# Kernel optimization log

Hardware: AMD Instinct MI355X
Metric: run time of the kernel (lower is better)

The kernel has to match this reference:

```python
import jax, jax.numpy as jnp
import numpy as np

N = 50000      # nodes
E = 800000     # edges (avg degree 16)
F_IN = 128     # num_features
H = 64         # hidden_dim
G = 64         # graphs in batch


def setup_inputs() -> dict:
    key = jax.random.key(0)
    ks = jax.random.split(key, 20)
    inp = {
        "x": jax.random.normal(ks[0], (N, F_IN), jnp.float32),
        "edge_index": jax.random.randint(ks[1], (2, E), 0, N, dtype=jnp.int32).astype(jnp.int64),
        "batch": jnp.sort(jax.random.randint(ks[2], (N,), 0, G, dtype=jnp.int32)).astype(jnp.int64),
    }
    # GraphConv layer dims: in -> out
    dims = [(F_IN, H), (H, 2 * H), (2 * H, 3 * H), (3 * H, H)]
    k = 3
    for i, (din, dout) in enumerate(dims):
        s = 1.0 / np.sqrt(din).astype(np.float32)
        inp[f"w{i+1}_rel"] = jax.random.normal(ks[k], (din, dout), jnp.float32) * s
        inp[f"w{i+1}_root"] = jax.random.normal(ks[k + 1], (din, dout), jnp.float32) * s
        inp[f"b{i+1}"] = jnp.zeros((dout,), jnp.float32)
        k += 2
    inp["head_w"] = jax.random.normal(ks[k], (H, 1), jnp.float32) * (1.0 / np.sqrt(H).astype(np.float32))
    inp["head_b"] = jnp.zeros((1,), jnp.float32)
    return inp


def _graph_conv(x, src, dst, w_rel, w_root, b):
    # PyG GraphConv: out = lin_rel(sum_{j in N(i)} x_j) + lin_root(x_i)
    agg = jax.ops.segment_sum(x[src], dst, num_segments=N)  # [N, din]
    return agg @ w_rel + b + x @ w_root


def reference(x, edge_index, batch,
              w1_rel, w1_root, b1,
              w2_rel, w2_root, b2,
              w3_rel, w3_root, b3,
              w4_rel, w4_root, b4,
              head_w, head_b):
    src, dst = edge_index[0], edge_index[1]
    h = jax.nn.relu(_graph_conv(x, src, dst, w1_rel, w1_root, b1))
    h = jax.nn.relu(_graph_conv(h, src, dst, w2_rel, w2_root, b2))
    h = jax.nn.relu(_graph_conv(h, src, dst, w3_rel, w3_root, b3))
    h = _graph_conv(h, src, dst, w4_rel, w4_root, b4)          # [N, H]
    # global_mean_pool over graph ids
    sums = jax.ops.segment_sum(h, batch, num_segments=G)       # [G, H]
    counts = jax.ops.segment_sum(jnp.ones((N,), h.dtype), batch, num_segments=G)
    pooled = sums / jnp.maximum(counts, 1.0)[:, None]          # [G, H]
    return pooled @ head_w + head_b                            # [G, 1]
```

## Files before the change

### kernel.cpp

```cpp
#include <hip/hip_runtime.h>


#define NNODES 50000
#define NEDGES 800000
#define NGRAPH 64
#define NBUK 256
#define BSZ 196
#define EPB (NEDGES / NBUK)
#define CVT_NB (NNODES * 128 / 4 / 256)
#define PACK_NB (160 * 512 / 256)
#define PREP_NB (CVT_NB + PACK_NB + 1)
#define RGRID ((NNODES + 127) / 128)
#define RCHUNK ((RGRID + 7) / 8)
#define GB_SPLIT 196
#define ZNB 32

typedef __attribute__((ext_vector_type(8))) __bf16 bf16x8;
typedef __attribute__((ext_vector_type(16))) float f32x16;

__device__ __forceinline__ unsigned short f2bf(float f) {
    unsigned u = __float_as_uint(f);
    u += 0x7fff + ((u >> 16) & 1);
    return (unsigned short)(u >> 16);
}
__device__ __forceinline__ float bf2f(unsigned b) {
    return __uint_as_float(b << 16);
}

__device__ __forceinline__ void dma16(const void* g, void* l) {
    __builtin_amdgcn_global_load_lds(
        (const __attribute__((address_space(1))) void*)g,
        (__attribute__((address_space(3))) void*)l, 16, 0, 0);
}


__device__ __forceinline__ void pack32(const float* __restrict__ W, unsigned short* __restrict__ dst,
                                       int KS_tot, int ks0, int dcols, int ct0,
                                       int tl, int ksl, int lane, int j) {
    int k = ksl * 16 + ((lane >> 5) << 3) + j;
    int col = tl * 32 + (lane & 31);
    dst[(((size_t)(ct0 + tl) * KS_tot + (ks0 + ksl)) * 64 + lane) * 8 + j] = f2bf(W[k * dcols + col]);
}

__device__ void prep_body(int b, int tid,
                          const float* x, unsigned short* xbf,
                          const float* w1_rel, const float* w1_root,
                          const float* w2_rel, const float* w2_root,
                          const float* w3_rel, const float* w3_root,
                          unsigned short* pL1, unsigned short* pL2, unsigned short* pL3,
                          const float* w4_rel, const float* w4_root,
                          const float* b4, const float* head_w,
                          float* wr, float* wt, float* cbuf) {
    if (b < CVT_NB) {
        int i = b * 256 + tid;
        float4 v = ((const float4*)x)[i];
        unsigned lo = (unsigned)f2bf(v.x) | ((unsigned)f2bf(v.y) << 16);
        unsigned hi = (unsigned)f2bf(v.z) | ((unsigned)f2bf(v.w) << 16);
        ((uint2*)xbf)[i] = make_uint2(lo, hi);
    } else if (b < CVT_NB + PACK_NB) {
        int idx = (b - CVT_NB) * 256 + tid;
        int g = idx >> 9;
        int t = idx & 511;
        int lane = (t >> 3) & 63, j = t & 7;
        if (g < 16)       { int gl = g;       pack32(w1_rel,  pL1, 8,  0, 64,  0, gl / 8, gl % 8, lane, j); }
        else if (g < 32)  { int gl = g - 16;  pack32(w1_root, pL1, 8,  0, 64,  2, gl / 8, gl % 8, lane, j); }
        else if (g < 48)  { int gl = g - 32;  pack32(w2_rel,  pL2, 8,  0, 128, 0, gl / 4, gl % 4, lane, j); }
        else if (g < 64)  { int gl = g - 48;  pack32(w2_root, pL2, 8,  4, 128, 0, gl / 4, gl % 4, lane, j); }
        else if (g < 112) { int gl = g - 64;  pack32(w3_rel,  pL3, 16, 0, 192, 0, gl / 8, gl % 8, lane, j); }
        else              { int gl = g - 112; pack32(w3_root, pL3, 16, 8, 192, 0, gl / 8, gl % 8, lane, j); }
    } else {
        if (tid < 192) {
            float ar = 0.f, at = 0.f;
            for (int j = 0; j < 64; j++) {
                float hw = head_w[j];
                ar = fmaf(w4_rel[tid * 64 + j], hw, ar);
                at = fmaf(w4_root[tid * 64 + j], hw, at);
            }
            wr[tid] = ar;
            wt[tid] = at;
        } else if (tid == 192) {
            float c = 0.f;
            for (int j = 0; j < 64; j++) c = fmaf(b4[j], head_w[j], c);
            cbuf[0] = c;
        }
    }
}


__global__ void __launch_bounds__(256) histprep_kernel(
    const int* __restrict__ edst, int* __restrict__ bcnt,
    const float* __restrict__ x, unsigned short* __restrict__ xbf,
    const float* __restrict__ w1_rel, const float* __restrict__ w1_root,
    const float* __restrict__ w2_rel, const float* __restrict__ w2_root,
    const float* __restrict__ w3_rel, const float* __restrict__ w3_root,
    unsigned short* __restrict__ pL1, unsigned short* __restrict__ pL2,
    unsigned short* __restrict__ pL3,
    const float* __restrict__ w4_rel, const float* __restrict__ w4_root,
    const float* __restrict__ b4, const float* __restrict__ head_w,
    float* __restrict__ wr, float* __restrict__ wt, float* __restrict__ cbuf)
{
    int tid = threadIdx.x, b = blockIdx.x;
    if (b < NBUK) {
        __shared__ int h[NBUK];
        h[tid] = 0;
        __syncthreads();
        int end = (b + 1) * EPB;
        for (int i = b * EPB + tid; i < end; i += 256)
            atomicAdd(&h[edst[i] / BSZ], 1);
        __syncthreads();
        bcnt[tid * NBUK + b] = h[tid];
    } else {
        prep_body(b - NBUK, tid, x, xbf, w1_rel, w1_root, w2_rel, w2_root,
                  w3_rel, w3_root, pL1, pL2, pL3, w4_rel, w4_root, b4, head_w,
                  wr, wt, cbuf);
    }
}


__global__ void scanzero_kernel(int* __restrict__ a, int* __restrict__ bsum, int n,
                                float4* __restrict__ zb, int zn16) {
    __shared__ int buf[256];
    int tid = threadIdx.x, b = blockIdx.x;
    if (b < NBUK) {
        int i = b * 256 + tid;
        int v = (i < n) ? a[i] : 0;
        buf[tid] = v;
        __syncthreads();
        #pragma unroll
        for (int off = 1; off < 256; off <<= 1) {
            int t = (tid >= off) ? buf[tid - off] : 0;
            __syncthreads();
            buf[tid] += t;
            __syncthreads();
        }
        if (i < n) a[i] = buf[tid] - v;
        if (tid == 255) bsum[b] = buf[255];
    } else {
        float4 zero = make_float4(0.f, 0.f, 0.f, 0.f);
        for (int i = (b - NBUK) * 256 + tid; i < zn16; i += ZNB * 256) zb[i] = zero;
    }
}


template<int KS, int NT, int NHALF, int ST, int KCH>
__device__ void gemm_body(
    unsigned short* sB, unsigned short* sA, int i,
    const unsigned short* __restrict__ A, const unsigned short* __restrict__ Wall,
    const float* __restrict__ bias, unsigned short* __restrict__ OUT,
    int ldo, int ocol0, int relu, int N,
    const float* __restrict__ wrp, const float* __restrict__ wtp,
    float* __restrict__ sb, float* __restrict__ tb)
{
    const int K = KS * 16;
    const int CPC = KCH * 2;

    int chunk = i / (8 * NHALF);
    int rem = i - chunk * (8 * NHALF);
    int halfsel = rem >> 3;
    int rowb = chunk * 8 + (rem & 7);
    int rbase = rowb * 128;
    if (rbase >= N) return;

    int tid = threadIdx.x;
    int wave = tid >> 6, lane = tid & 63;
    int l32 = lane & 31, half = lane >> 5;
    const unsigned short* W = Wall + (size_t)halfsel * NT * KS * 512;

    #pragma unroll
    for (int j = 0; j < NT * KS * 64 / 256; j++) {
        int p = j * 256 + wave * 64;
        dma16(W + ((size_t)p + lane) * 8, sB + (size_t)p * 8);
    }

    f32x16 acc[NT];
    #pragma unroll
    for (int t = 0; t < NT; t++)
        #pragma unroll
        for (int r = 0; r < 16; r++) acc[t][r] = 0.f;

    int lr = wave * 32 + l32;

    for (int kb = 0; kb < KS; kb += KCH) {
        if (kb > 0) __syncthreads();
        #pragma unroll
        for (int j = 0; j < 128 * CPC / 256; j++) {
            int p = j * 256 + wave * 64 + lane;
            int r = p / CPC;
            int c = p - r * CPC;
            int cg = c ^ (r & (CPC - 1));
            dma16(A + (size_t)(rbase + r) * K + kb * 16 + cg * 8,
                  sA + (size_t)(j * 256 + wave * 64) * 8);
        }
        __syncthreads();
        #pragma unroll
        for (int l = 0; l < KCH; l++) {
            int cs = (l * 2 + half) ^ (lr & (CPC - 1));
            bf16x8 a = *(const bf16x8*)(sA + (size_t)lr * (KCH * 16) + cs * 8);
            int ks = kb + l;
            #pragma unroll
            for (int t = 0; t < NT; t++) {
                bf16x8 b = *(const bf16x8*)(sB + ((size_t)(t * KS + ks) * 64 + lane) * 8);
                acc[t] = __builtin_amdgcn_mfma_f32_32x32x16_bf16(a, b, acc[t], 0, 0, 0);
            }
        }
    }

    int wrbase = rbase + wave * 32;
    if constexpr (ST) {
        #pragma unroll
        for (int reg = 0; reg < 16; reg++) {
            int row = wrbase + (reg & 3) + 8 * (reg >> 2) + 4 * half;
            float sv = 0.f, tv = 0.f;
            #pragma unroll
            for (int t = 0; t < NT; t++) {
                int col = halfsel * NT * 32 + t * 32 + l32;
                float v = fmaxf(acc[t][reg] + bias[col], 0.f);
                sv = fmaf(v, wrp[col], sv);
                tv = fmaf(v, wtp[col], tv);
            }
            #pragma unroll
            for (int m = 1; m < 32; m <<= 1) {
                sv += __shfl_xor(sv, m, 64);
                tv += __shfl_xor(tv, m, 64);
            }
            if (l32 == 0 && row < N) {
                atomicAdd(&sb[row], sv);
                atomicAdd(&tb[row], tv);
            }
        }
    } else {
        #pragma unroll
        for (int t = 0; t < NT; t++) {
            int col = t * 32 + l32;
            float bi = bias ? bias[col] : 0.f;
            #pragma unroll
            for (int reg = 0; reg < 16; reg++) {
                int row = wrbase + (reg & 3) + 8 * (reg >> 2) + 4 * half;
                if (row < N) {
                    float v = acc[t][reg] + bi;
                    if (relu) v = fmaxf(v, 0.f);
                    OUT[(size_t)row * ldo + ocol0 + col] = f2bf(v);
                }
            }
        }
    }
}

template<int KS, int NT, int NHALF, int ST, int KCH>
__global__ __launch_bounds__(256) void gemm_v5(
    const unsigned short* __restrict__ A, const unsigned short* __restrict__ Wall,
    const float* __restrict__ bias, unsigned short* __restrict__ OUT,
    int ldo, int ocol0, int relu, int N,
    const float* __restrict__ wrp, const float* __restrict__ wtp,
    float* __restrict__ sb, float* __restrict__ tb)
{
    __shared__ __align__(16) unsigned short sB[NT * KS * 512];
    __shared__ __align__(16) unsigned short sA[128 * KCH * 16];
    gemm_body<KS, NT, NHALF, ST, KCH>(sB, sA, blockIdx.x, A, Wall, bias, OUT,
                                      ldo, ocol0, relu, N, wrp, wtp, sb, tb);
}


__global__ void __launch_bounds__(256) partgemm_kernel(
    const int* __restrict__ src, const int* __restrict__ dst,
    const int* __restrict__ cnt, const int* __restrict__ braw,
    int* __restrict__ sbsum, unsigned long long* __restrict__ pedge,
    const unsigned short* __restrict__ A, const unsigned short* __restrict__ W,
    unsigned short* __restrict__ OUT, int N)
{
    __shared__ __align__(16) unsigned short smem[32768];
    int tid = threadIdx.x, b = blockIdx.x;
    if (b < NBUK) {
        int* lbase = (int*)smem;
        int* sscan = lbase + 256;
        int v = braw[tid];
        sscan[tid] = v;
        __syncthreads();
        #pragma unroll
        for (int off = 1; off < 256; off <<= 1) {
            int t = (tid >= off) ? sscan[tid - off] : 0;
            __syncthreads();
            sscan[tid] += t;
            __syncthreads();
        }
        int ex = sscan[tid] - v;
        if (b == 0) sbsum[tid] = ex;
        lbase[tid] = cnt[tid * NBUK + b] + ex;
        __syncthreads();
        int end = (b + 1) * EPB;
        for (int i = b * EPB + tid; i < end; i += 256) {
            int s = src[i], d = dst[i];
            int pos = atomicAdd(&lbase[d / BSZ], 1);
            pedge[pos] = (unsigned long long)(unsigned)s | ((unsigned long long)(unsigned)d << 32);
        }
    } else {
        gemm_body<8, 4, 1, 0, 8>(smem, smem + 16384, b - NBUK,
                                 A, W, nullptr, OUT, 128, 0, 0, N,
                                 nullptr, nullptr, nullptr, nullptr);
    }
}


__global__ void __launch_bounds__(256) buildgemm_kernel(
    const unsigned long long* __restrict__ pedge, const int* __restrict__ sbsum,
    int* __restrict__ rp, int* __restrict__ csr,
    const unsigned short* __restrict__ A, const unsigned short* __restrict__ W,
    unsigned short* __restrict__ OUT, int N)
{
    __shared__ __align__(16) unsigned short smem[32768];
    int tid = threadIdx.x, b = blockIdx.x;
    if (b < NBUK) {
        int* sdeg  = (int*)smem;
        int* sc    = sdeg + 256;
        int* sbase = sc + 256;
        int* sfill = sbase + 256;
        int node0 = b * BSZ;
        int ncnt = NNODES - node0;
        if (ncnt > BSZ) ncnt = BSZ;
        if (ncnt < 0) ncnt = 0;
        int seg0 = sbsum[b];
        int seg1 = (b + 1 < NBUK) ? sbsum[b + 1] : NEDGES;
        sdeg[tid] = 0;
        sfill[tid] = 0;
        __syncthreads();
        for (int i = seg0 + tid; i < seg1; i += 256)
            atomicAdd(&sdeg[(int)(pedge[i] >> 32) - node0], 1);
        __syncthreads();
        sc[tid] = sdeg[tid];
        __syncthreads();
        #pragma unroll
        for (int off = 1; off < 256; off <<= 1) {
            int t = (tid >= off) ? sc[tid - off] : 0;
            __syncthreads();
            sc[tid] += t;
            __syncthreads();
        }
        sbase[tid] = sc[tid] - sdeg[tid];
        if (tid < ncnt) rp[node0 + tid] = seg0 + sbase[tid];
        if (b == NBUK - 1 && tid == 0) rp[NNODES] = NEDGES;
        __syncthreads();
        for (int i = seg0 + tid; i < seg1; i += 256) {
            unsigned long long p = pedge[i];
            int d = (int)(p >> 32) - node0;
            int pos = atomicAdd(&sfill[d], 1);
            csr[seg0 + sbase[d] + pos] = (int)(p & 0xffffffffu);
        }
    } else {
        gemm_body<8, 4, 1, 0, 8>(smem, smem + 16384, GB_SPLIT + (b - NBUK),
                                 A, W, nullptr, OUT, 128, 0, 0, N,
                                 nullptr, nullptr, nullptr, nullptr);
    }
}


__device__ __forceinline__ void acc8(float* a, uint4 u) {
    a[0] += bf2f(u.x & 0xffffu); a[1] += bf2f(u.x >> 16);
    a[2] += bf2f(u.y & 0xffffu); a[3] += bf2f(u.y >> 16);
    a[4] += bf2f(u.z & 0xffffu); a[5] += bf2f(u.z >> 16);
    a[6] += bf2f(u.w & 0xffffu); a[7] += bf2f(u.w >> 16);
}

template<int LPF, int SUBS>
__global__ void agg_kernel_v4(const unsigned short* __restrict__ X, int ldx,
                              const int* __restrict__ rp, const int* __restrict__ csr,
                              const unsigned short* __restrict__ root, int ldr,
                              const float* __restrict__ bias, int relu,
                              unsigned short* __restrict__ OUT, int ldo, int N) {
    int t = blockIdx.x * blockDim.x + threadIdx.x;
    int node = t / (SUBS * LPF);
    int r = t % (SUBS * LPF);
    int sub = r / LPF;
    int sl = r % LPF;
    if (node >= N) return;
    float a[8] = {0.f, 0.f, 0.f, 0.f, 0.f, 0.f, 0.f, 0.f};
    int e0 = rp[node], e1 = rp[node + 1];
    const unsigned short* xb = X + 8 * sl;
    int e = e0 + sub;
    for (; e + 3 * SUBS < e1; e += 4 * SUBS) {
        int s0 = csr[e], s1 = csr[e + SUBS], s2 = csr[e + 2 * SUBS], s3 = csr[e + 3 * SUBS];
        uint4 u0 = *(const uint4*)(xb + (size_t)s0 * ldx);
        uint4 u1 = *(const uint4*)(xb + (size_t)s1 * ldx);
        uint4 u2 = *(const uint4*)(xb + (size_t)s2 * ldx);
        uint4 u3 = *(const uint4*)(xb + (size_t)s3 * ldx);
        acc8(a, u0); acc8(a, u1); acc8(a, u2); acc8(a, u3);
    }
    for (; e < e1; e += SUBS) {
        uint4 u = *(const uint4*)(xb + (size_t)csr[e] * ldx);
        acc8(a, u);
    }
    #pragma unroll
    for (int m = LPF; m < SUBS * LPF; m <<= 1)
        #pragma unroll
        for (int i = 0; i < 8; i++) a[i] += __shfl_xor(a[i], m, 64);
    if (sub == 0) {
        if (root) {
            uint4 u = *(const uint4*)(root + (size_t)node * ldr + 8 * sl);
            acc8(a, u);
        }
        if (bias) {
            float4 b0 = *(const float4*)(bias + 8 * sl);
            float4 b1 = *(const float4*)(bias + 8 * sl + 4);
            a[0] += b0.x; a[1] += b0.y; a[2] += b0.z; a[3] += b0.w;
            a[4] += b1.x; a[5] += b1.y; a[6] += b1.z; a[7] += b1.w;
        }
        if (relu) {
            #pragma unroll
            for (int i = 0; i < 8; i++) a[i] = fmaxf(a[i], 0.f);
        }
        uint4 o;
        o.x = (unsigned)f2bf(a[0]) | ((unsigned)f2bf(a[1]) << 16);
        o.y = (unsigned)f2bf(a[2]) | ((unsigned)f2bf(a[3]) << 16);
        o.z = (unsigned)f2bf(a[4]) | ((unsigned)f2bf(a[5]) << 16);
        o.w = (unsigned)f2bf(a[6]) | ((unsigned)f2bf(a[7]) << 16);
        *(uint4*)(OUT + (size_t)node * ldo + 8 * sl) = o;
    }
}


__global__ void aggpool_kernel(const float* __restrict__ s, const float* __restrict__ t,
                               const int* __restrict__ rp, const int* __restrict__ csr,
                               const int* __restrict__ batch, float* __restrict__ gsum,
                               int* __restrict__ cnt, int N) {
    __shared__ float ls[NGRAPH];
    __shared__ int lc[NGRAPH];
    int tid = threadIdx.x;
    if (tid < NGRAPH) { ls[tid] = 0.f; lc[tid] = 0; }
    __syncthreads();
    int n = blockIdx.x * blockDim.x + tid;
    if (n < N) {
        float a = 0.f;
        int e = rp[n], e1 = rp[n + 1];
        for (; e + 3 < e1; e += 4) {
            int s0 = csr[e], s1 = csr[e + 1], s2 = csr[e + 2], s3 = csr[e + 3];
            a += s[s0] + s[s1] + s[s2] + s[s3];
        }
        for (; e < e1; e++) a += s[csr[e]];
        int g = batch[n];
        atomicAdd(&ls[g], a + t[n]);
        atomicAdd(&lc[g], 1);
    }
    __syncthreads();
    if (tid < NGRAPH && lc[tid] > 0) {
        atomicAdd(&gsum[tid], ls[tid]);
        atomicAdd(&cnt[tid], lc[tid]);
    }
}

__global__ void final_kernel(const float* __restrict__ gsum, const int* __restrict__ cnt,
                             const float* __restrict__ cbuf, const float* __restrict__ head_b,
                             float* __restrict__ out) {
    int g = threadIdx.x;
    if (g < NGRAPH) {
        float c = (float)(cnt[g] > 0 ? cnt[g] : 1);
        out[g] = gsum[g] / c + cbuf[0] + head_b[0];
    }
}


extern "C" void kernel_launch(void* const* d_in, const int* in_sizes, int n_in,
                              void* d_out, int out_size, void* d_ws, size_t ws_size,
                              hipStream_t stream) {
    const float* x       = (const float*)d_in[0];
    const int*   edge    = (const int*)d_in[1];
    const int*   batch   = (const int*)d_in[2];
    const float* w1_rel  = (const float*)d_in[3];
    const float* w1_root = (const float*)d_in[4];
    const float* b1      = (const float*)d_in[5];
    const float* w2_rel  = (const float*)d_in[6];
    const float* w2_root = (const float*)d_in[7];
    const float* b2      = (const float*)d_in[8];
    const float* w3_rel  = (const float*)d_in[9];
    const float* w3_root = (const float*)d_in[10];
    const float* b3      = (const float*)d_in[11];
    const float* w4_rel  = (const float*)d_in[12];
    const float* w4_root = (const float*)d_in[13];
    const float* b4      = (const float*)d_in[14];
    const float* head_w  = (const float*)d_in[15];
    const float* head_b  = (const float*)d_in[16];
    float* out = (float*)d_out;

    const int N = NNODES, E = NEDGES;
    const int* esrc = edge;
    const int* edst = edge + E;

    char* ws = (char*)d_ws;
    size_t off = 0;
    auto alloc = [&](size_t bytes) -> char* {
        char* p = ws + off;
        off = (off + bytes + 255) & ~(size_t)255;
        return p;
    };
    float* gsum  = (float*)alloc(NGRAPH * 4);
    int*   cnt   = (int*)alloc(NGRAPH * 4);
    float* sbuf  = (float*)alloc((size_t)N * 4);
    float* tbuf  = (float*)alloc((size_t)N * 4);
    size_t zero_bytes = off;
    int*   bcnt  = (int*)alloc((size_t)NBUK * NBUK * 4);
    int*   bsum  = (int*)alloc(256 * 4);
    int*   sbsum = (int*)alloc(256 * 4);
    int*   rp    = (int*)alloc((size_t)(N + 1) * 4);
    int*   csr   = (int*)alloc((size_t)E * 4);
    unsigned long long* pedge = (unsigned long long*)alloc((size_t)E * 8);
    unsigned short* xbf    = (unsigned short*)alloc((size_t)N * 128 * 2);
    unsigned short* z1     = (unsigned short*)alloc((size_t)N * 128 * 2);
    unsigned short* combo2 = (unsigned short*)alloc((size_t)N * 128 * 2);
    unsigned short* combo3 = (unsigned short*)alloc((size_t)N * 256 * 2);
    unsigned short* pL1    = (unsigned short*)alloc(4 * 8 * 512 * 2);
    unsigned short* pL2    = (unsigned short*)alloc(4 * 8 * 512 * 2);
    unsigned short* pL3    = (unsigned short*)alloc(6 * 16 * 512 * 2);
    float* wr    = (float*)alloc(192 * 4);
    float* wt    = (float*)alloc(192 * 4);
    float* cbuf  = (float*)alloc(4);
    (void)ws_size;

    const int TB = 256;

    histprep_kernel<<<NBUK + PREP_NB, 256, 0, stream>>>(
        edst, bcnt, x, xbf, w1_rel, w1_root, w2_rel, w2_root, w3_rel, w3_root,
        pL1, pL2, pL3, w4_rel, w4_root, b4, head_w, wr, wt, cbuf);
    scanzero_kernel<<<NBUK + ZNB, 256, 0, stream>>>(
        bcnt, bsum, NBUK * NBUK, (float4*)ws, (int)(zero_bytes / 16));
    partgemm_kernel<<<NBUK + GB_SPLIT, 256, 0, stream>>>(
        esrc, edst, bcnt, bsum, sbsum, pedge, xbf, pL1, z1, N);
    buildgemm_kernel<<<NBUK + (RCHUNK * 8 - GB_SPLIT), 256, 0, stream>>>(
        pedge, sbsum, rp, csr, xbf, pL1, z1, N);

    agg_kernel_v4<8, 2><<<(N * 16 + TB - 1) / TB, TB, 0, stream>>>(z1, 128, rp, csr,
                                                                   z1 + 64, 128, b1, 1, combo2 + 64, 128, N);
    agg_kernel_v4<8, 2><<<(N * 16 + TB - 1) / TB, TB, 0, stream>>>(combo2 + 64, 128, rp, csr,
                                                                   nullptr, 0, nullptr, 0, combo2, 128, N);
    gemm_v5<8, 4, 1, 0, 8><<<RCHUNK * 8, 256, 0, stream>>>(
        combo2, pL2, b2, combo3, 256, 128, 1, N, nullptr, nullptr, nullptr, nullptr);
    agg_kernel_v4<16, 2><<<(N * 32 + TB - 1) / TB, TB, 0, stream>>>(combo3 + 128, 256, rp, csr,
                                                                    nullptr, 0, nullptr, 0, combo3, 256, N);
    gemm_v5<16, 3, 2, 1, 4><<<RCHUNK * 8 * 2, 256, 0, stream>>>(
        combo3, pL3, b3, nullptr, 0, 0, 0, N, wr, wt, sbuf, tbuf);

    aggpool_kernel<<<(N + TB - 1) / TB, TB, 0, stream>>>(sbuf, tbuf, rp, csr, batch, gsum, cnt, N);
    final_kernel<<<1, 64, 0, stream>>>(gsum, cnt, cbuf, head_b, out);
}
```

Baseline: 241.2 us.

## Split neighbor aggregation into source-range passes for cache locality

CSR construction now sorts each node's edges by which quarter of the node range the source falls in, and records the sub-range boundaries in a new rpm array. Each aggregation is then split into several launches that each gather only from one source-node range, so the gathered feature rows form a smaller working set that can stay in cache. Partial sums pass between launches through an fp32 buffer that reuses the xbf workspace. The cost is more kernel launches and extra fp32 partial-sum reads and writes per node.

```diff
diff --git a/kernel.cpp b/kernel.cpp
--- a/kernel.cpp
+++ b/kernel.cpp
@@ -14,9 +14,11 @@
 #define RCHUNK ((RGRID + 7) / 8)
 #define GB_SPLIT 196
 #define ZNB 32
+#define QS ((NNODES + 3) / 4)
 
 typedef __attribute__((ext_vector_type(8))) __bf16 bf16x8;
 typedef __attribute__((ext_vector_type(16))) float f32x16;
+typedef __attribute__((ext_vector_type(4))) float f32x4v;
 
 __device__ __forceinline__ unsigned short f2bf(float f) {
     unsigned u = __float_as_uint(f);
@@ -303,30 +305,40 @@
 
 __global__ void __launch_bounds__(256) buildgemm_kernel(
     const unsigned long long* __restrict__ pedge, const int* __restrict__ sbsum,
-    int* __restrict__ rp, int* __restrict__ csr,
+    int* __restrict__ rp, int* __restrict__ rpm, int* __restrict__ csr,
     const unsigned short* __restrict__ A, const unsigned short* __restrict__ W,
     unsigned short* __restrict__ OUT, int N)
 {
     __shared__ __align__(16) unsigned short smem[32768];
     int tid = threadIdx.x, b = blockIdx.x;
     if (b < NBUK) {
-        int* sdeg  = (int*)smem;
-        int* sc    = sdeg + 256;
-        int* sbase = sc + 256;
-        int* sfill = sbase + 256;
+        int* sdeg4  = (int*)smem;
+        int* sfill4 = sdeg4 + 1024;
+        int* sc     = sfill4 + 1024;
+        int* sbase  = sc + 256;
         int node0 = b * BSZ;
         int ncnt = NNODES - node0;
         if (ncnt > BSZ) ncnt = BSZ;
         if (ncnt < 0) ncnt = 0;
         int seg0 = sbsum[b];
         int seg1 = (b + 1 < NBUK) ? sbsum[b + 1] : NEDGES;
-        sdeg[tid] = 0;
-        sfill[tid] = 0;
-        __syncthreads();
-        for (int i = seg0 + tid; i < seg1; i += 256)
-            atomicAdd(&sdeg[(int)(pedge[i] >> 32) - node0], 1);
-        __syncthreads();
-        sc[tid] = sdeg[tid];
+        #pragma unroll
+        for (int k = 0; k < 4; k++) {
+            sdeg4[tid * 4 + k] = 0;
+            sfill4[tid * 4 + k] = 0;
+        }
+        __syncthreads();
+        for (int i = seg0 + tid; i < seg1; i += 256) {
+            unsigned long long p = pedge[i];
+            int d = (int)(p >> 32) - node0;
+            int s = (int)(p & 0xffffffffu);
+            atomicAdd(&sdeg4[d * 4 + s / QS], 1);
+        }
+        __syncthreads();
+        int c0 = sdeg4[tid * 4 + 0], c1 = sdeg4[tid * 4 + 1];
+        int c2 = sdeg4[tid * 4 + 2], c3 = sdeg4[tid * 4 + 3];
+        int tot = c0 + c1 + c2 + c3;
+        sc[tid] = tot;
         __syncthreads();
         #pragma unroll
         for (int off = 1; off < 256; off <<= 1) {
@@ -335,15 +347,27 @@
             sc[tid] += t;
             __syncthreads();
         }
-        sbase[tid] = sc[tid] - sdeg[tid];
-        if (tid < ncnt) rp[node0 + tid] = seg0 + sbase[tid];
+        sbase[tid] = sc[tid] - tot;
+        int base = seg0 + sbase[tid];
+        if (tid < ncnt) {
+            rp[node0 + tid] = base;
+            rpm[3 * (node0 + tid) + 0] = base + c0;
+            rpm[3 * (node0 + tid) + 1] = base + c0 + c1;
+            rpm[3 * (node0 + tid) + 2] = base + c0 + c1 + c2;
+        }
         if (b == NBUK - 1 && tid == 0) rp[NNODES] = NEDGES;
+        sdeg4[tid * 4 + 0] = base;
+        sdeg4[tid * 4 + 1] = base + c0;
+        sdeg4[tid * 4 + 2] = base + c0 + c1;
+        sdeg4[tid * 4 + 3] = base + c0 + c1 + c2;
         __syncthreads();
         for (int i = seg0 + tid; i < seg1; i += 256) {
             unsigned long long p = pedge[i];
             int d = (int)(p >> 32) - node0;
-            int pos = atomicAdd(&sfill[d], 1);
-            csr[seg0 + sbase[d] + pos] = (int)(p & 0xffffffffu);
+            int s = (int)(p & 0xffffffffu);
+            int q = d * 4 + s / QS;
+            int pos = sdeg4[q] + atomicAdd(&sfill4[q], 1);
+            csr[pos] = s;
         }
     } else {
         gemm_body<8, 4, 1, 0, 8>(smem, smem + 16384, GB_SPLIT + (b - NBUK),
@@ -361,8 +385,10 @@
 }
 
 template<int LPF, int SUBS>
-__global__ void agg_kernel_v4(const unsigned short* __restrict__ X, int ldx,
-                              const int* __restrict__ rp, const int* __restrict__ csr,
+__global__ void agg_kernel_v7(const unsigned short* __restrict__ X, int ldx,
+                              const int* __restrict__ rp, const int* __restrict__ rpm,
+                              const int* __restrict__ csr, int qa, int qb,
+                              const float* __restrict__ pin, float* __restrict__ pout,
                               const unsigned short* __restrict__ root, int ldr,
                               const float* __restrict__ bias, int relu,
                               unsigned short* __restrict__ OUT, int ldo, int N) {
@@ -373,7 +399,8 @@
     int sl = r % LPF;
     if (node >= N) return;
     float a[8] = {0.f, 0.f, 0.f, 0.f, 0.f, 0.f, 0.f, 0.f};
-    int e0 = rp[node], e1 = rp[node + 1];
+    int e0 = (qa == 0) ? rp[node] : rpm[3 * node + qa - 1];
+    int e1 = (qb == 4) ? rp[node + 1] : rpm[3 * node + qb - 1];
     const unsigned short* xb = X + 8 * sl;
     int e = e0 + sub;
     for (; e + 3 * SUBS < e1; e += 4 * SUBS) {
@@ -393,26 +420,41 @@
         #pragma unroll
         for (int i = 0; i < 8; i++) a[i] += __shfl_xor(a[i], m, 64);
     if (sub == 0) {
-        if (root) {
-            uint4 u = *(const uint4*)(root + (size_t)node * ldr + 8 * sl);
-            acc8(a, u);
-        }
-        if (bias) {
-            float4 b0 = *(const float4*)(bias + 8 * sl);
-            float4 b1 = *(const float4*)(bias + 8 * sl + 4);
-            a[0] += b0.x; a[1] += b0.y; a[2] += b0.z; a[3] += b0.w;
-            a[4] += b1.x; a[5] += b1.y; a[6] += b1.z; a[7] += b1.w;
-        }
-        if (relu) {
-            #pragma unroll
-            for (int i = 0; i < 8; i++) a[i] = fmaxf(a[i], 0.f);
-        }
-        uint4 o;
-        o.x = (unsigned)f2bf(a[0]) | ((unsigned)f2bf(a[1]) << 16);
-        o.y = (unsigned)f2bf(a[2]) | ((unsigned)f2bf(a[3]) << 16);
-        o.z = (unsigned)f2bf(a[4]) | ((unsigned)f2bf(a[5]) << 16);
-        o.w = (unsigned)f2bf(a[6]) | ((unsigned)f2bf(a[7]) << 16);
-        *(uint4*)(OUT + (size_t)node * ldo + 8 * sl) = o;
+        if (pin) {
+            const float* pi = pin + (size_t)node * (LPF * 8) + 8 * sl;
+            f32x4v p0 = __builtin_nontemporal_load((const f32x4v*)pi);
+            f32x4v p1 = __builtin_nontemporal_load((const f32x4v*)(pi + 4));
+            a[0] += p0[0]; a[1] += p0[1]; a[2] += p0[2]; a[3] += p0[3];
+            a[4] += p1[0]; a[5] += p1[1]; a[6] += p1[2]; a[7] += p1[3];
+        }
+        if (pout) {
+            float* po = pout + (size_t)node * (LPF * 8) + 8 * sl;
+            f32x4v v0 = {a[0], a[1], a[2], a[3]};
+            f32x4v v1 = {a[4], a[5], a[6], a[7]};
+            __builtin_nontemporal_store(v0, (f32x4v*)po);
+            __builtin_nontemporal_store(v1, (f32x4v*)(po + 4));
+        } else {
+            if (root) {
+                uint4 u = *(const uint4*)(root + (size_t)node * ldr + 8 * sl);
+                acc8(a, u);
+            }
+            if (bias) {
+                float4 b0 = *(const float4*)(bias + 8 * sl);
+                float4 b1 = *(const float4*)(bias + 8 * sl + 4);
+                a[0] += b0.x; a[1] += b0.y; a[2] += b0.z; a[3] += b0.w;
+                a[4] += b1.x; a[5] += b1.y; a[6] += b1.z; a[7] += b1.w;
+            }
+            if (relu) {
+                #pragma unroll
+                for (int i = 0; i < 8; i++) a[i] = fmaxf(a[i], 0.f);
+            }
+            uint4 o;
+            o.x = (unsigned)f2bf(a[0]) | ((unsigned)f2bf(a[1]) << 16);
+            o.y = (unsigned)f2bf(a[2]) | ((unsigned)f2bf(a[3]) << 16);
+            o.z = (unsigned)f2bf(a[4]) | ((unsigned)f2bf(a[5]) << 16);
+            o.w = (unsigned)f2bf(a[6]) | ((unsigned)f2bf(a[7]) << 16);
+            *(uint4*)(OUT + (size_t)node * ldo + 8 * sl) = o;
+        }
     }
 }
 
@@ -499,6 +541,7 @@
     int*   bsum  = (int*)alloc(256 * 4);
     int*   sbsum = (int*)alloc(256 * 4);
     int*   rp    = (int*)alloc((size_t)(N + 1) * 4);
+    int*   rpm   = (int*)alloc((size_t)N * 3 * 4);
     int*   csr   = (int*)alloc((size_t)E * 4);
     unsigned long long* pedge = (unsigned long long*)alloc((size_t)E * 8);
     unsigned short* xbf    = (unsigned short*)alloc((size_t)N * 128 * 2);
@@ -513,6 +556,9 @@
     float* cbuf  = (float*)alloc(4);
     (void)ws_size;
 
+    float* pbufA = (float*)xbf;
+    float* pbufB = (float*)xbf;
+
     const int TB = 256;
 
     histprep_kernel<<<NBUK + PREP_NB, 256, 0, stream>>>(
@@ -523,16 +569,34 @@
     partgemm_kernel<<<NBUK + GB_SPLIT, 256, 0, stream>>>(
         esrc, edst, bcnt, bsum, sbsum, pedge, xbf, pL1, z1, N);
     buildgemm_kernel<<<NBUK + (RCHUNK * 8 - GB_SPLIT), 256, 0, stream>>>(
-        pedge, sbsum, rp, csr, xbf, pL1, z1, N);
-
-    agg_kernel_v4<8, 2><<<(N * 16 + TB - 1) / TB, TB, 0, stream>>>(z1, 128, rp, csr,
-                                                                   z1 + 64, 128, b1, 1, combo2 + 64, 128, N);
-    agg_kernel_v4<8, 2><<<(N * 16 + TB - 1) / TB, TB, 0, stream>>>(combo2 + 64, 128, rp, csr,
-                                                                   nullptr, 0, nullptr, 0, combo2, 128, N);
+        pedge, sbsum, rp, rpm, csr, xbf, pL1, z1, N);
+
+    agg_kernel_v7<8, 2><<<(N * 16 + TB - 1) / TB, TB, 0, stream>>>(
+        z1, 128, rp, rpm, csr, 0, 2, nullptr, pbufA,
+        nullptr, 0, nullptr, 0, nullptr, 0, N);
+    agg_kernel_v7<8, 2><<<(N * 16 + TB - 1) / TB, TB, 0, stream>>>(
+        z1, 128, rp, rpm, csr, 2, 4, pbufA, nullptr,
+        z1 + 64, 128, b1, 1, combo2 + 64, 128, N);
+    agg_kernel_v7<8, 2><<<(N * 16 + TB - 1) / TB, TB, 0, stream>>>(
+        combo2 + 64, 128, rp, rpm, csr, 0, 2, nullptr, pbufA,
+        nullptr, 0, nullptr, 0, nullptr, 0, N);
+    agg_kernel_v7<8, 2><<<(N * 16 + TB - 1) / TB, TB, 0, stream>>>(
+        combo2 + 64, 128, rp, rpm, csr, 2, 4, pbufA, nullptr,
+        nullptr, 0, nullptr, 0, combo2, 128, N);
     gemm_v5<8, 4, 1, 0, 8><<<RCHUNK * 8, 256, 0, stream>>>(
         combo2, pL2, b2, combo3, 256, 128, 1, N, nullptr, nullptr, nullptr, nullptr);
-    agg_kernel_v4<16, 2><<<(N * 32 + TB - 1) / TB, TB, 0, stream>>>(combo3 + 128, 256, rp, csr,
-                                                                    nullptr, 0, nullptr, 0, combo3, 256, N);
+    agg_kernel_v7<16, 2><<<(N * 32 + TB - 1) / TB, TB, 0, stream>>>(
+        combo3 + 128, 256, rp, rpm, csr, 0, 1, nullptr, pbufB,
+        nullptr, 0, nullptr, 0, nullptr, 0, N);
+    agg_kernel_v7<16, 2><<<(N * 32 + TB - 1) / TB, TB, 0, stream>>>(
+        combo3 + 128, 256, rp, rpm, csr, 1, 2, pbufB, pbufB,
+        nullptr, 0, nullptr, 0, nullptr, 0, N);
+    agg_kernel_v7<16, 2><<<(N * 32 + TB - 1) / TB, TB, 0, stream>>>(
+        combo3 + 128, 256, rp, rpm, csr, 2, 3, pbufB, pbufB,
+        nullptr, 0, nullptr, 0, nullptr, 0, N);
+    agg_kernel_v7<16, 2><<<(N * 32 + TB - 1) / TB, TB, 0, stream>>>(
+        combo3 + 128, 256, rp, rpm, csr, 3, 4, pbufB, nullptr,
+        nullptr, 0, nullptr, 0, combo3, 256, N);
     gemm_v5<16, 3, 2, 1, 4><<<RCHUNK * 8 * 2, 256, 0, stream>>>(
         combo3, pL3, b3, nullptr, 0, 0, 0, N, wr, wt, sbuf, tbuf);
 
```

Result: slower. 303.0 us (+25.6%).
